# Kernel tuning notes

Hardware: AMD Instinct MI355X
Metric: run time of the kernel (lower is better)

The kernel has to match this reference:

```python
import jax, jax.numpy as jnp
import numpy as np

N_NODES = 100000
N_EDGES = 1600000
IN_FEATS = 128
HIDDEN = 128
NUM_CLASSES = 4


def setup_inputs() -> dict:
    key = jax.random.key(0)
    ks = jax.random.split(key, 8)
    features = jax.random.normal(ks[0], (N_NODES, IN_FEATS), dtype=jnp.float32)
    src = jax.random.randint(ks[1], (N_EDGES,), 0, N_NODES, dtype=jnp.int64)
    dst = jax.random.randint(ks[2], (N_EDGES,), 0, N_NODES, dtype=jnp.int64)
    s = 1.0 / np.sqrt(IN_FEATS)
    W1 = jax.random.normal(ks[3], (IN_FEATS, HIDDEN), dtype=jnp.float32) * s
    b1 = jnp.zeros((HIDDEN,), dtype=jnp.float32)
    W2 = jax.random.normal(ks[4], (HIDDEN, HIDDEN), dtype=jnp.float32) * s
    b2 = jnp.zeros((HIDDEN,), dtype=jnp.float32)
    Wc = jax.random.normal(ks[5], (HIDDEN, NUM_CLASSES), dtype=jnp.float32) * s
    bc = jnp.zeros((NUM_CLASSES,), dtype=jnp.float32)
    return {"features": features, "src": src, "dst": dst,
            "W1": W1, "b1": b1, "W2": W2, "b2": b2, "Wc": Wc, "bc": bc}


def _graph_conv(x, W, b, src, dst, n_nodes, activation=True):
    # DGL GraphConv, norm='both': D_out^{-1/2} A^T D_in... i.e. symmetric norm.
    ones = jnp.ones((src.shape[0],), dtype=x.dtype)
    deg_out = jnp.clip(jax.ops.segment_sum(ones, src, num_segments=n_nodes), 1.0)
    deg_in = jnp.clip(jax.ops.segment_sum(ones, dst, num_segments=n_nodes), 1.0)
    # scale sources, project (in >= out so matmul first, math-equivalent), gather-scatter
    h = (x * (deg_out ** -0.5)[:, None]) @ W            # [N, out]
    msg = h[src]                                         # [E, out] gather
    agg = jax.ops.segment_sum(msg, dst, num_segments=n_nodes)  # [N, out] scatter-add
    h = agg * (deg_in ** -0.5)[:, None] + b
    return jax.nn.relu(h) if activation else h


def reference(features, src, dst, W1, b1, W2, b2, Wc, bc):
    # eval-mode forward: dropout is identity
    n = features.shape[0]
    h = _graph_conv(features, W1, b1, src, dst, n, activation=True)
    h = _graph_conv(h, W2, b2, src, dst, n, activation=True)
    return h @ Wc + bc  # [N, num_classes] logits
```

## Files before the change

kernel.cpp:

```cpp
#include <hip/hip_runtime.h>
#include <hip/hip_fp16.h>
#include <math.h>

#define N_NODES 100000
#define N_EDGES 1600000
#define F 128
#define NBUK 196
#define BSH 9
#define BSZ 512
#define CAP 10240
#define NPART 392

typedef _Float16 half8 __attribute__((ext_vector_type(8)));
typedef float    f32x4 __attribute__((ext_vector_type(4)));
typedef int      i32x4 __attribute__((ext_vector_type(4)));

__global__ __launch_bounds__(256) void init_pack(int* __restrict__ curD,
                                                 int* __restrict__ curS,
                                                 _Float16* __restrict__ padrow,
                                                 const float* __restrict__ W1,
                                                 const float* __restrict__ W2,
                                                 _Float16* __restrict__ hi1,
                                                 _Float16* __restrict__ lo1,
                                                 _Float16* __restrict__ hi2,
                                                 _Float16* __restrict__ lo2)
{
    int t = threadIdx.x;
    if (blockIdx.x == 0) {
        if (t < NBUK) { curD[t] = t * CAP; curS[t] = t * CAP; }
        if (t < 16) reinterpret_cast<int4*>(padrow)[t] = make_int4(0, 0, 0, 0);
        return;
    }
    int gidx = (blockIdx.x - 1) * 256 + t;
    const float* W = (gidx < 16384) ? W1 : W2;
    _Float16* hi = (gidx < 16384) ? hi1 : hi2;
    _Float16* lo = (gidx < 16384) ? lo1 : lo2;
    int idx = gidx & 16383;
    int f = idx >> 9, r = idx & 511;
    int l = r >> 3, j = r & 7;
    int kc = f >> 3, ct = f & 7;
    int k = kc * 32 + (l >> 4) * 8 + j;
    int n = ct * 16 + (l & 15);
    float w = W[k * 128 + n];
    _Float16 h = (_Float16)w;
    hi[idx] = h;
    lo[idx] = (_Float16)(w - (float)h);
}

__global__ __launch_bounds__(512) void part_gemm1(const int* __restrict__ src,
                                                  const int* __restrict__ dst,
                                                  int* __restrict__ curD,
                                                  int* __restrict__ curS,
                                                  int* __restrict__ bukD,
                                                  unsigned short* __restrict__ bukS,
                                                  const float* __restrict__ X,
                                                  const _Float16* __restrict__ Whi,
                                                  const _Float16* __restrict__ Wlo,
                                                  _Float16* __restrict__ Y, int N)
{
    __shared__ int hd[NBUK], hs[NBUK], bd[NBUK], bs[NBUK], cd[NBUK], cs[NBUK];
    const int tid = threadIdx.x;

    if (blockIdx.x < NPART) {
        const int chunk = (((N_EDGES + NPART - 1) / NPART) + 3) & ~3;
        const int beg = blockIdx.x * chunk;
        const int end = min(beg + chunk, N_EDGES);
        if (beg >= end) return;
        if (tid < NBUK) { hd[tid] = 0; hs[tid] = 0; cd[tid] = 0; cs[tid] = 0; }
        __syncthreads();
        const int b4 = beg >> 2, e4 = end >> 2;
        const int i0 = b4 + tid, i1 = i0 + 512;
        const bool v0 = i0 < e4, v1 = i1 < e4;
        i32x4 d0 = {}, s0 = {}, d1 = {}, s1 = {};
        if (v0) {
            d0 = reinterpret_cast<const i32x4*>(dst)[i0];
            s0 = reinterpret_cast<const i32x4*>(src)[i0];
            atomicAdd(&hd[d0.x >> BSH], 1); atomicAdd(&hd[d0.y >> BSH], 1);
            atomicAdd(&hd[d0.z >> BSH], 1); atomicAdd(&hd[d0.w >> BSH], 1);
            atomicAdd(&hs[s0.x >> BSH], 1); atomicAdd(&hs[s0.y >> BSH], 1);
            atomicAdd(&hs[s0.z >> BSH], 1); atomicAdd(&hs[s0.w >> BSH], 1);
        }
        if (v1) {
            d1 = reinterpret_cast<const i32x4*>(dst)[i1];
            s1 = reinterpret_cast<const i32x4*>(src)[i1];
            atomicAdd(&hd[d1.x >> BSH], 1); atomicAdd(&hd[d1.y >> BSH], 1);
            atomicAdd(&hd[d1.z >> BSH], 1); atomicAdd(&hd[d1.w >> BSH], 1);
            atomicAdd(&hs[s1.x >> BSH], 1); atomicAdd(&hs[s1.y >> BSH], 1);
            atomicAdd(&hs[s1.z >> BSH], 1); atomicAdd(&hs[s1.w >> BSH], 1);
        }
        __syncthreads();
        if (tid < NBUK) {
            bd[tid] = hd[tid] ? atomicAdd(&curD[tid], hd[tid]) : 0;
            bs[tid] = hs[tid] ? atomicAdd(&curS[tid], hs[tid]) : 0;
        }
        __syncthreads();
        if (v0) {
            int dd[4] = { d0.x, d0.y, d0.z, d0.w };
            int ss[4] = { s0.x, s0.y, s0.z, s0.w };
            #pragma unroll
            for (int j = 0; j < 4; j++) {
                int bin = dd[j] >> BSH;
                int r = atomicAdd(&cd[bin], 1);
                bukD[bd[bin] + r] = ((dd[j] & 511) << 17) | ss[j];
                int bin2 = ss[j] >> BSH;
                int r2 = atomicAdd(&cs[bin2], 1);
                bukS[bs[bin2] + r2] = (unsigned short)(ss[j] & 511);
            }
        }
        if (v1) {
            int dd[4] = { d1.x, d1.y, d1.z, d1.w };
            int ss[4] = { s1.x, s1.y, s1.z, s1.w };
            #pragma unroll
            for (int j = 0; j < 4; j++) {
                int bin = dd[j] >> BSH;
                int r = atomicAdd(&cd[bin], 1);
                bukD[bd[bin] + r] = ((dd[j] & 511) << 17) | ss[j];
                int bin2 = ss[j] >> BSH;
                int r2 = atomicAdd(&cs[bin2], 1);
                bukS[bs[bin2] + r2] = (unsigned short)(ss[j] & 511);
            }
        }
        return;
    }

    const int l = tid & 63, w = tid >> 6;
    const int quad = l >> 4, m = l & 15;
    const int row0 = (blockIdx.x - NPART) * 256;
    const half8* Bh = reinterpret_cast<const half8*>(Whi);
    const half8* Bl = reinterpret_cast<const half8*>(Wlo);

    f32x4 acc[2][8] = {};

    for (int kc = 0; kc < 4; kc++) {
        half8 ah[2];
        #pragma unroll
        for (int rt = 0; rt < 2; rt++) {
            int grow = row0 + w * 32 + rt * 16 + m;
            float4 xa = make_float4(0.f, 0.f, 0.f, 0.f), xb = xa;
            if (grow < N) {
                const float4* Xp = reinterpret_cast<const float4*>(X) + (size_t)grow * 32 + kc * 8 + quad * 2;
                xa = Xp[0]; xb = Xp[1];
            }
            ah[rt][0] = (_Float16)xa.x; ah[rt][1] = (_Float16)xa.y;
            ah[rt][2] = (_Float16)xa.z; ah[rt][3] = (_Float16)xa.w;
            ah[rt][4] = (_Float16)xb.x; ah[rt][5] = (_Float16)xb.y;
            ah[rt][6] = (_Float16)xb.z; ah[rt][7] = (_Float16)xb.w;
        }
        #pragma unroll
        for (int ct = 0; ct < 8; ct++) {
            int f = kc * 8 + ct;
            half8 bh = Bh[f * 64 + l];
            half8 bl = Bl[f * 64 + l];
            #pragma unroll
            for (int rt = 0; rt < 2; rt++) {
                acc[rt][ct] = __builtin_amdgcn_mfma_f32_16x16x32_f16(ah[rt], bh, acc[rt][ct], 0, 0, 0);
                acc[rt][ct] = __builtin_amdgcn_mfma_f32_16x16x32_f16(ah[rt], bl, acc[rt][ct], 0, 0, 0);
            }
        }
    }

    #pragma unroll
    for (int rt = 0; rt < 2; rt++) {
        #pragma unroll
        for (int r = 0; r < 4; r++) {
            int grow = row0 + w * 32 + rt * 16 + quad * 4 + r;
            if (grow < N) {
                #pragma unroll
                for (int ct = 0; ct < 8; ct++)
                    Y[(size_t)grow * 128 + ct * 16 + m] = (_Float16)(acc[rt][ct][r]);
            }
        }
    }
}

__global__ __launch_bounds__(512) void deg_out(const unsigned short* __restrict__ bukS,
                                               const int* __restrict__ curS,
                                               float* __restrict__ sout)
{
    __shared__ int h[BSZ];
    const int tid = threadIdx.x;
    const int n0 = blockIdx.x << BSH;
    const int lo = blockIdx.x * CAP, hi = curS[blockIdx.x];
    const int cnt = hi - lo;
    h[tid] = 0;
    __syncthreads();
    const uint4* p8 = reinterpret_cast<const uint4*>(bukS + lo);
    const int nv = cnt >> 3;
    for (int j = tid; j < nv; j += 512) {
        uint4 v = p8[j];
        atomicAdd(&h[v.x & 0xFFFF], 1); atomicAdd(&h[v.x >> 16], 1);
        atomicAdd(&h[v.y & 0xFFFF], 1); atomicAdd(&h[v.y >> 16], 1);
        atomicAdd(&h[v.z & 0xFFFF], 1); atomicAdd(&h[v.z >> 16], 1);
        atomicAdd(&h[v.w & 0xFFFF], 1); atomicAdd(&h[v.w >> 16], 1);
    }
    for (int i = lo + (nv << 3) + tid; i < hi; i += 512)
        atomicAdd(&h[bukS[i]], 1);
    __syncthreads();
    int node = n0 + tid;
    if (node < N_NODES) sout[node] = rsqrtf((float)max(h[tid], 1));
}

__global__ __launch_bounds__(512) void csr_wv(const int* __restrict__ bukD,
                                              const int* __restrict__ curD,
                                              const float* __restrict__ sout,
                                              int* __restrict__ row_ptr,
                                              float* __restrict__ sin_,
                                              int* __restrict__ col,
                                              float* __restrict__ wv)
{
    __shared__ int h[BSZ], sc[BSZ], cur[BSZ];
    const int tid = threadIdx.x;
    const int n0 = blockIdx.x << BSH;
    const int lo = blockIdx.x * CAP, hi = curD[blockIdx.x];
    const int cnt = hi - lo;
    h[tid] = 0;
    __syncthreads();
    const i32x4* p4 = reinterpret_cast<const i32x4*>(bukD + lo);
    const int nv = cnt >> 2;
    for (int j = tid; j < nv; j += 512) {
        i32x4 v = p4[j];
        atomicAdd(&h[((unsigned)v.x) >> 17], 1);
        atomicAdd(&h[((unsigned)v.y) >> 17], 1);
        atomicAdd(&h[((unsigned)v.z) >> 17], 1);
        atomicAdd(&h[((unsigned)v.w) >> 17], 1);
    }
    for (int i = lo + (nv << 2) + tid; i < hi; i += 512)
        atomicAdd(&h[((unsigned)bukD[i]) >> 17], 1);
    __syncthreads();
    int own = h[tid];
    int own4 = (own + 3) & ~3;
    sc[tid] = own4;
    __syncthreads();
    for (int off = 1; off < 512; off <<= 1) {
        int u = (tid >= off) ? sc[tid - off] : 0;
        __syncthreads();
        sc[tid] += u;
        __syncthreads();
    }
    int ex = sc[tid] - own4;
    cur[tid] = ex;
    int node = n0 + tid;
    if (node < N_NODES) {
        row_ptr[2 * node]     = lo + ex;
        row_ptr[2 * node + 1] = lo + ex + own4;
        sin_[node] = rsqrtf((float)max(own, 1));
    }
    __syncthreads();
    for (int j = tid; j < nv; j += 512) {
        i32x4 v = p4[j];
        int pv[4] = { v.x, v.y, v.z, v.w };
        #pragma unroll
        for (int q = 0; q < 4; q++) {
            int p = pv[q];
            int s = p & 0x1FFFF;
            int r = atomicAdd(&cur[((unsigned)p) >> 17], 1);
            col[lo + r] = s;
            wv[lo + r]  = sout[s];
        }
    }
    for (int i = lo + (nv << 2) + tid; i < hi; i += 512) {
        int p = bukD[i];
        int s = p & 0x1FFFF;
        int r = atomicAdd(&cur[((unsigned)p) >> 17], 1);
        col[lo + r] = s;
        wv[lo + r]  = sout[s];
    }
    for (int k = own; k < own4; k++) {
        col[lo + ex + k] = N_NODES;
        wv[lo + ex + k]  = 0.f;
    }
}

#define ACCW(vv, ww) \
    a0 = fmaf(ww, (float)vv[0], a0); a1 = fmaf(ww, (float)vv[1], a1); \
    a2 = fmaf(ww, (float)vv[2], a2); a3 = fmaf(ww, (float)vv[3], a3); \
    a4 = fmaf(ww, (float)vv[4], a4); a5 = fmaf(ww, (float)vv[5], a5); \
    a6 = fmaf(ww, (float)vv[6], a6); a7 = fmaf(ww, (float)vv[7], a7);

#define ACCU(vv) \
    a0 += (float)vv[0]; a1 += (float)vv[1]; a2 += (float)vv[2]; a3 += (float)vv[3]; \
    a4 += (float)vv[4]; a5 += (float)vv[5]; a6 += (float)vv[6]; a7 += (float)vv[7];

__global__ __launch_bounds__(256) void gather_agg_s(const _Float16* __restrict__ Hh,
                                                    const int* __restrict__ row_ptr,
                                                    const int* __restrict__ col,
                                                    const float* __restrict__ wv,
                                                    const float* __restrict__ sin_,
                                                    const float* __restrict__ bias,
                                                    _Float16* __restrict__ Yh, int N)
{
    const int sub  = threadIdx.x & 15;
    const int node = blockIdx.x * 16 + (threadIdx.x >> 4);
    if (node >= N) return;
    const int beg = row_ptr[2 * node], end = row_ptr[2 * node + 1];
    const half8* __restrict__ H8 = reinterpret_cast<const half8*>(Hh);

    float a0 = 0.f, a1 = 0.f, a2 = 0.f, a3 = 0.f, a4 = 0.f, a5 = 0.f, a6 = 0.f, a7 = 0.f;
    int i = beg;
    for (; i + 8 <= end; i += 8) {
        int4 ca = *reinterpret_cast<const int4*>(col + i);
        int4 cb = *reinterpret_cast<const int4*>(col + i + 4);
        float4 wa = *reinterpret_cast<const float4*>(wv + i);
        float4 wb = *reinterpret_cast<const float4*>(wv + i + 4);
        half8 v0 = H8[((size_t)ca.x << 4) | sub];
        half8 v1 = H8[((size_t)ca.y << 4) | sub];
        half8 v2 = H8[((size_t)ca.z << 4) | sub];
        half8 v3 = H8[((size_t)ca.w << 4) | sub];
        half8 v4 = H8[((size_t)cb.x << 4) | sub];
        half8 v5 = H8[((size_t)cb.y << 4) | sub];
        half8 v6 = H8[((size_t)cb.z << 4) | sub];
        half8 v7 = H8[((size_t)cb.w << 4) | sub];
        ACCW(v0, wa.x) ACCW(v1, wa.y) ACCW(v2, wa.z) ACCW(v3, wa.w)
        ACCW(v4, wb.x) ACCW(v5, wb.y) ACCW(v6, wb.z) ACCW(v7, wb.w)
    }
    if (i < end) {
        int4 ca = *reinterpret_cast<const int4*>(col + i);
        float4 wa = *reinterpret_cast<const float4*>(wv + i);
        half8 v0 = H8[((size_t)ca.x << 4) | sub];
        half8 v1 = H8[((size_t)ca.y << 4) | sub];
        half8 v2 = H8[((size_t)ca.z << 4) | sub];
        half8 v3 = H8[((size_t)ca.w << 4) | sub];
        ACCW(v0, wa.x) ACCW(v1, wa.y) ACCW(v2, wa.z) ACCW(v3, wa.w)
    }
    float scn = sin_[node];
    const float4* B4 = reinterpret_cast<const float4*>(bias);
    float4 bA = B4[2 * sub], bB = B4[2 * sub + 1];
    half8 o;
    o[0] = (_Float16)fmaxf(fmaf(a0, scn, bA.x), 0.f);
    o[1] = (_Float16)fmaxf(fmaf(a1, scn, bA.y), 0.f);
    o[2] = (_Float16)fmaxf(fmaf(a2, scn, bA.z), 0.f);
    o[3] = (_Float16)fmaxf(fmaf(a3, scn, bA.w), 0.f);
    o[4] = (_Float16)fmaxf(fmaf(a4, scn, bB.x), 0.f);
    o[5] = (_Float16)fmaxf(fmaf(a5, scn, bB.y), 0.f);
    o[6] = (_Float16)fmaxf(fmaf(a6, scn, bB.z), 0.f);
    o[7] = (_Float16)fmaxf(fmaf(a7, scn, bB.w), 0.f);
    reinterpret_cast<half8*>(Yh)[(size_t)node * 16 + sub] = o;
}

__global__ __launch_bounds__(256) void gather_cls(const _Float16* __restrict__ Hh,
                                                  const int* __restrict__ row_ptr,
                                                  const int* __restrict__ col,
                                                  const float* __restrict__ sin_,
                                                  const float* __restrict__ bias,
                                                  const float* __restrict__ Wc,
                                                  const float* __restrict__ bc,
                                                  float* __restrict__ out, int N)
{
    __shared__ float4 Wcs[128];
    for (int t = threadIdx.x; t < 128; t += 256)
        Wcs[t] = reinterpret_cast<const float4*>(Wc)[t];
    __syncthreads();

    const int sub  = threadIdx.x & 15;
    const int node = blockIdx.x * 16 + (threadIdx.x >> 4);
    if (node >= N) return;
    const int beg = row_ptr[2 * node], end = row_ptr[2 * node + 1];
    const half8* __restrict__ H8 = reinterpret_cast<const half8*>(Hh);

    float a0 = 0.f, a1 = 0.f, a2 = 0.f, a3 = 0.f, a4 = 0.f, a5 = 0.f, a6 = 0.f, a7 = 0.f;
    int i = beg;
    for (; i + 8 <= end; i += 8) {
        int4 ca = *reinterpret_cast<const int4*>(col + i);
        int4 cb = *reinterpret_cast<const int4*>(col + i + 4);
        half8 v0 = H8[((size_t)ca.x << 4) | sub];
        half8 v1 = H8[((size_t)ca.y << 4) | sub];
        half8 v2 = H8[((size_t)ca.z << 4) | sub];
        half8 v3 = H8[((size_t)ca.w << 4) | sub];
        half8 v4 = H8[((size_t)cb.x << 4) | sub];
        half8 v5 = H8[((size_t)cb.y << 4) | sub];
        half8 v6 = H8[((size_t)cb.z << 4) | sub];
        half8 v7 = H8[((size_t)cb.w << 4) | sub];
        ACCU(v0) ACCU(v1) ACCU(v2) ACCU(v3)
        ACCU(v4) ACCU(v5) ACCU(v6) ACCU(v7)
    }
    if (i < end) {
        int4 ca = *reinterpret_cast<const int4*>(col + i);
        half8 v0 = H8[((size_t)ca.x << 4) | sub];
        half8 v1 = H8[((size_t)ca.y << 4) | sub];
        half8 v2 = H8[((size_t)ca.z << 4) | sub];
        half8 v3 = H8[((size_t)ca.w << 4) | sub];
        ACCU(v0) ACCU(v1) ACCU(v2) ACCU(v3)
    }
    float scn = sin_[node];
    const float4* B4 = reinterpret_cast<const float4*>(bias);
    float4 bA = B4[2 * sub], bB = B4[2 * sub + 1];
    float h0 = fmaxf(fmaf(a0, scn, bA.x), 0.f);
    float h1 = fmaxf(fmaf(a1, scn, bA.y), 0.f);
    float h2 = fmaxf(fmaf(a2, scn, bA.z), 0.f);
    float h3 = fmaxf(fmaf(a3, scn, bA.w), 0.f);
    float h4 = fmaxf(fmaf(a4, scn, bB.x), 0.f);
    float h5 = fmaxf(fmaf(a5, scn, bB.y), 0.f);
    float h6 = fmaxf(fmaf(a6, scn, bB.z), 0.f);
    float h7 = fmaxf(fmaf(a7, scn, bB.w), 0.f);

    float lx = 0.f, ly = 0.f, lz = 0.f, lw = 0.f;
    float4 w;
    w = Wcs[sub * 8 + 0]; lx = fmaf(h0, w.x, lx); ly = fmaf(h0, w.y, ly); lz = fmaf(h0, w.z, lz); lw = fmaf(h0, w.w, lw);
    w = Wcs[sub * 8 + 1]; lx = fmaf(h1, w.x, lx); ly = fmaf(h1, w.y, ly); lz = fmaf(h1, w.z, lz); lw = fmaf(h1, w.w, lw);
    w = Wcs[sub * 8 + 2]; lx = fmaf(h2, w.x, lx); ly = fmaf(h2, w.y, ly); lz = fmaf(h2, w.z, lz); lw = fmaf(h2, w.w, lw);
    w = Wcs[sub * 8 + 3]; lx = fmaf(h3, w.x, lx); ly = fmaf(h3, w.y, ly); lz = fmaf(h3, w.z, lz); lw = fmaf(h3, w.w, lw);
    w = Wcs[sub * 8 + 4]; lx = fmaf(h4, w.x, lx); ly = fmaf(h4, w.y, ly); lz = fmaf(h4, w.z, lz); lw = fmaf(h4, w.w, lw);
    w = Wcs[sub * 8 + 5]; lx = fmaf(h5, w.x, lx); ly = fmaf(h5, w.y, ly); lz = fmaf(h5, w.z, lz); lw = fmaf(h5, w.w, lw);
    w = Wcs[sub * 8 + 6]; lx = fmaf(h6, w.x, lx); ly = fmaf(h6, w.y, ly); lz = fmaf(h6, w.z, lz); lw = fmaf(h6, w.w, lw);
    w = Wcs[sub * 8 + 7]; lx = fmaf(h7, w.x, lx); ly = fmaf(h7, w.y, ly); lz = fmaf(h7, w.z, lz); lw = fmaf(h7, w.w, lw);

    #pragma unroll
    for (int m = 1; m < 16; m <<= 1) {
        lx += __shfl_xor(lx, m);
        ly += __shfl_xor(ly, m);
        lz += __shfl_xor(lz, m);
        lw += __shfl_xor(lw, m);
    }
    if (sub == 0) {
        float4 bcv = reinterpret_cast<const float4*>(bc)[0];
        float4 r;
        r.x = lx + bcv.x; r.y = ly + bcv.y; r.z = lz + bcv.z; r.w = lw + bcv.w;
        reinterpret_cast<float4*>(out)[node] = r;
    }
}

__global__ __launch_bounds__(256) void gemm_mfma_f16(const _Float16* __restrict__ Xh,
                                                     const _Float16* __restrict__ Whi,
                                                     const _Float16* __restrict__ Wlo,
                                                     const float* __restrict__ srow,
                                                     _Float16* __restrict__ Y, int N)
{
    const int tid = threadIdx.x;
    const int l = tid & 63, w = tid >> 6;
    const int quad = l >> 4, m = l & 15;
    const int row0 = blockIdx.x * 128;
    const half8* Bh = reinterpret_cast<const half8*>(Whi);
    const half8* Bl = reinterpret_cast<const half8*>(Wlo);

    f32x4 acc[2][8] = {};

    for (int kc = 0; kc < 4; kc++) {
        half8 a[2];
        #pragma unroll
        for (int rt = 0; rt < 2; rt++) {
            int grow = row0 + w * 32 + rt * 16 + m;
            half8 z = {};
            a[rt] = (grow < N)
                ? *reinterpret_cast<const half8*>(Xh + (size_t)grow * 128 + kc * 32 + quad * 8)
                : z;
        }
        #pragma unroll
        for (int ct = 0; ct < 8; ct++) {
            int f = kc * 8 + ct;
            half8 bh = Bh[f * 64 + l];
            half8 bl = Bl[f * 64 + l];
            #pragma unroll
            for (int rt = 0; rt < 2; rt++) {
                acc[rt][ct] = __builtin_amdgcn_mfma_f32_16x16x32_f16(a[rt], bh, acc[rt][ct], 0, 0, 0);
                acc[rt][ct] = __builtin_amdgcn_mfma_f32_16x16x32_f16(a[rt], bl, acc[rt][ct], 0, 0, 0);
            }
        }
    }

    #pragma unroll
    for (int rt = 0; rt < 2; rt++) {
        #pragma unroll
        for (int r = 0; r < 4; r++) {
            int grow = row0 + w * 32 + rt * 16 + quad * 4 + r;
            if (grow < N) {
                float s = srow[grow];
                #pragma unroll
                for (int ct = 0; ct < 8; ct++)
                    Y[(size_t)grow * 128 + ct * 16 + m] = (_Float16)(acc[rt][ct][r] * s);
            }
        }
    }
}

extern "C" void kernel_launch(void* const* d_in, const int* in_sizes, int n_in,
                              void* d_out, int out_size, void* d_ws, size_t ws_size,
                              hipStream_t stream)
{
    const float* features = (const float*)d_in[0];
    const int*   src      = (const int*)d_in[1];
    const int*   dst      = (const int*)d_in[2];
    const float* W1       = (const float*)d_in[3];
    const float* b1       = (const float*)d_in[4];
    const float* W2       = (const float*)d_in[5];
    const float* b2       = (const float*)d_in[6];
    const float* Wc       = (const float*)d_in[7];
    const float* bc       = (const float*)d_in[8];
    float* out = (float*)d_out;

    char* ws = (char*)d_ws;
    const size_t MB = 1 << 20;
    int* curD  = (int*)(ws + 0);
    int* curS  = (int*)(ws + 1024);
    _Float16* Whi1 = (_Float16*)(ws + 64 * 1024);
    _Float16* Wlo1 = (_Float16*)(ws + 96 * 1024);
    _Float16* Whi2 = (_Float16*)(ws + 128 * 1024);
    _Float16* Wlo2 = (_Float16*)(ws + 160 * 1024);
    float* sout    = (float*)(ws + 512 * 1024);
    float* sin_    = (float*)(ws + 1 * MB);
    int*   row_ptr = (int*)(ws + 2 * MB);
    int*   col     = (int*)(ws + 3 * MB);
    float* wv      = (float*)(ws + 11 * MB);
    _Float16* hMsg = (_Float16*)(ws + 25 * MB);
    int*   bukD    = (int*)(ws + 52 * MB);
    unsigned short* bukS = (unsigned short*)(ws + 60 * MB);
    _Float16* hA   = (_Float16*)(ws + 52 * MB);

    const int N = N_NODES;
    const int NGB = (N + 15) / 16;

    init_pack<<<129, 256, 0, stream>>>(curD, curS, hMsg + (size_t)N * F,
                                       W1, W2, Whi1, Wlo1, Whi2, Wlo2);

    part_gemm1<<<NPART + 391, 512, 0, stream>>>(src, dst, curD, curS, bukD, bukS,
                                                features, Whi1, Wlo1, hMsg, N);

    deg_out<<<NBUK, 512, 0, stream>>>(bukS, curS, sout);

    csr_wv<<<NBUK, 512, 0, stream>>>(bukD, curD, sout, row_ptr, sin_, col, wv);

    gather_agg_s<<<NGB, 256, 0, stream>>>(hMsg, row_ptr, col, wv, sin_, b1, hA, N);

    gemm_mfma_f16<<<(N + 127) / 128, 256, 0, stream>>>(hA, Whi2, Wlo2, sout, hMsg, N);
    gather_cls<<<NGB, 256, 0, stream>>>(hMsg, row_ptr, col, sin_, b2, Wc, bc, out, N);
}
```

Baseline: 305.6 us.

## Fuse layer-1 gather aggregation with layer-2 MFMA GEMM; double partition blocks

The layer-1 gather/aggregate kernel now stages each block's 16 aggregated fp16 rows in shared memory and immediately multiplies them by W2 using split hi/lo fp16 MFMA. This drops the separate GEMM kernel and the global write and read of the intermediate activation. The partition phase also doubles its block count so each block handles one int4 edge vector per thread instead of two, for more parallelism in bucketing. The cost is that each small block reloads the W2 fragments, and the node-count bounds checks are removed on the assumption that N is a multiple of 16.

After: 294.5 us. 1.04x faster.

```diff
diff --git a/kernel.cpp b/kernel.cpp
--- a/kernel.cpp
+++ b/kernel.cpp
@@ -9,7 +9,7 @@
 #define BSH 9
 #define BSZ 512
 #define CAP 10240
-#define NPART 392
+#define NPART 784
 
 typedef _Float16 half8 __attribute__((ext_vector_type(8)));
 typedef float    f32x4 __attribute__((ext_vector_type(4)));
@@ -17,7 +17,8 @@
 
 __global__ __launch_bounds__(256) void init_pack(int* __restrict__ curD,
                                                  int* __restrict__ curS,
-                                                 _Float16* __restrict__ padrow,
+                                                 _Float16* __restrict__ padrow1,
+                                                 _Float16* __restrict__ padrow2,
                                                  const float* __restrict__ W1,
                                                  const float* __restrict__ W2,
                                                  _Float16* __restrict__ hi1,
@@ -28,7 +29,8 @@
     int t = threadIdx.x;
     if (blockIdx.x == 0) {
         if (t < NBUK) { curD[t] = t * CAP; curS[t] = t * CAP; }
-        if (t < 16) reinterpret_cast<int4*>(padrow)[t] = make_int4(0, 0, 0, 0);
+        if (t < 16) reinterpret_cast<int4*>(padrow1)[t] = make_int4(0, 0, 0, 0);
+        else if (t >= 32 && t < 48) reinterpret_cast<int4*>(padrow2)[t - 32] = make_int4(0, 0, 0, 0);
         return;
     }
     int gidx = (blockIdx.x - 1) * 256 + t;
@@ -69,9 +71,9 @@
         if (tid < NBUK) { hd[tid] = 0; hs[tid] = 0; cd[tid] = 0; cs[tid] = 0; }
         __syncthreads();
         const int b4 = beg >> 2, e4 = end >> 2;
-        const int i0 = b4 + tid, i1 = i0 + 512;
-        const bool v0 = i0 < e4, v1 = i1 < e4;
-        i32x4 d0 = {}, s0 = {}, d1 = {}, s1 = {};
+        const int i0 = b4 + tid;
+        const bool v0 = i0 < e4;
+        i32x4 d0 = {}, s0 = {};
         if (v0) {
             d0 = reinterpret_cast<const i32x4*>(dst)[i0];
             s0 = reinterpret_cast<const i32x4*>(src)[i0];
@@ -80,14 +82,6 @@
             atomicAdd(&hs[s0.x >> BSH], 1); atomicAdd(&hs[s0.y >> BSH], 1);
             atomicAdd(&hs[s0.z >> BSH], 1); atomicAdd(&hs[s0.w >> BSH], 1);
         }
-        if (v1) {
-            d1 = reinterpret_cast<const i32x4*>(dst)[i1];
-            s1 = reinterpret_cast<const i32x4*>(src)[i1];
-            atomicAdd(&hd[d1.x >> BSH], 1); atomicAdd(&hd[d1.y >> BSH], 1);
-            atomicAdd(&hd[d1.z >> BSH], 1); atomicAdd(&hd[d1.w >> BSH], 1);
-            atomicAdd(&hs[s1.x >> BSH], 1); atomicAdd(&hs[s1.y >> BSH], 1);
-            atomicAdd(&hs[s1.z >> BSH], 1); atomicAdd(&hs[s1.w >> BSH], 1);
-        }
         __syncthreads();
         if (tid < NBUK) {
             bd[tid] = hd[tid] ? atomicAdd(&curD[tid], hd[tid]) : 0;
@@ -97,19 +91,6 @@
         if (v0) {
             int dd[4] = { d0.x, d0.y, d0.z, d0.w };
             int ss[4] = { s0.x, s0.y, s0.z, s0.w };
-            #pragma unroll
-            for (int j = 0; j < 4; j++) {
-                int bin = dd[j] >> BSH;
-                int r = atomicAdd(&cd[bin], 1);
-                bukD[bd[bin] + r] = ((dd[j] & 511) << 17) | ss[j];
-                int bin2 = ss[j] >> BSH;
-                int r2 = atomicAdd(&cs[bin2], 1);
-                bukS[bs[bin2] + r2] = (unsigned short)(ss[j] & 511);
-            }
-        }
-        if (v1) {
-            int dd[4] = { d1.x, d1.y, d1.z, d1.w };
-            int ss[4] = { s1.x, s1.y, s1.z, s1.w };
             #pragma unroll
             for (int j = 0; j < 4; j++) {
                 int bin = dd[j] >> BSH;
@@ -281,17 +262,22 @@
     a0 += (float)vv[0]; a1 += (float)vv[1]; a2 += (float)vv[2]; a3 += (float)vv[3]; \
     a4 += (float)vv[4]; a5 += (float)vv[5]; a6 += (float)vv[6]; a7 += (float)vv[7];
 
-__global__ __launch_bounds__(256) void gather_agg_s(const _Float16* __restrict__ Hh,
+__global__ __launch_bounds__(256) void gather_gemm2(const _Float16* __restrict__ Hh,
                                                     const int* __restrict__ row_ptr,
                                                     const int* __restrict__ col,
                                                     const float* __restrict__ wv,
                                                     const float* __restrict__ sin_,
                                                     const float* __restrict__ bias,
-                                                    _Float16* __restrict__ Yh, int N)
-{
-    const int sub  = threadIdx.x & 15;
-    const int node = blockIdx.x * 16 + (threadIdx.x >> 4);
-    if (node >= N) return;
+                                                    const _Float16* __restrict__ Whi,
+                                                    const _Float16* __restrict__ Wlo,
+                                                    const float* __restrict__ sout,
+                                                    _Float16* __restrict__ Y)
+{
+    __shared__ _Float16 At[16][128];
+    const int tid = threadIdx.x;
+    const int sub  = tid & 15;
+    const int g0   = tid >> 4;
+    const int node = blockIdx.x * 16 + g0;
     const int beg = row_ptr[2 * node], end = row_ptr[2 * node + 1];
     const half8* __restrict__ H8 = reinterpret_cast<const half8*>(Hh);
 
@@ -322,19 +308,52 @@
         half8 v3 = H8[((size_t)ca.w << 4) | sub];
         ACCW(v0, wa.x) ACCW(v1, wa.y) ACCW(v2, wa.z) ACCW(v3, wa.w)
     }
-    float scn = sin_[node];
-    const float4* B4 = reinterpret_cast<const float4*>(bias);
-    float4 bA = B4[2 * sub], bB = B4[2 * sub + 1];
-    half8 o;
-    o[0] = (_Float16)fmaxf(fmaf(a0, scn, bA.x), 0.f);
-    o[1] = (_Float16)fmaxf(fmaf(a1, scn, bA.y), 0.f);
-    o[2] = (_Float16)fmaxf(fmaf(a2, scn, bA.z), 0.f);
-    o[3] = (_Float16)fmaxf(fmaf(a3, scn, bA.w), 0.f);
-    o[4] = (_Float16)fmaxf(fmaf(a4, scn, bB.x), 0.f);
-    o[5] = (_Float16)fmaxf(fmaf(a5, scn, bB.y), 0.f);
-    o[6] = (_Float16)fmaxf(fmaf(a6, scn, bB.z), 0.f);
-    o[7] = (_Float16)fmaxf(fmaf(a7, scn, bB.w), 0.f);
-    reinterpret_cast<half8*>(Yh)[(size_t)node * 16 + sub] = o;
+    {
+        float scn = sin_[node];
+        const float4* B4 = reinterpret_cast<const float4*>(bias);
+        float4 bA = B4[2 * sub], bB = B4[2 * sub + 1];
+        half8 o;
+        o[0] = (_Float16)fmaxf(fmaf(a0, scn, bA.x), 0.f);
+        o[1] = (_Float16)fmaxf(fmaf(a1, scn, bA.y), 0.f);
+        o[2] = (_Float16)fmaxf(fmaf(a2, scn, bA.z), 0.f);
+        o[3] = (_Float16)fmaxf(fmaf(a3, scn, bA.w), 0.f);
+        o[4] = (_Float16)fmaxf(fmaf(a4, scn, bB.x), 0.f);
+        o[5] = (_Float16)fmaxf(fmaf(a5, scn, bB.y), 0.f);
+        o[6] = (_Float16)fmaxf(fmaf(a6, scn, bB.z), 0.f);
+        o[7] = (_Float16)fmaxf(fmaf(a7, scn, bB.w), 0.f);
+        *reinterpret_cast<half8*>(&At[g0][sub * 8]) = o;
+    }
+    __syncthreads();
+
+    const int l = tid & 63, w = tid >> 6;
+    const int quad = l >> 4, m = l & 15;
+    const half8* Bh = reinterpret_cast<const half8*>(Whi);
+    const half8* Bl = reinterpret_cast<const half8*>(Wlo);
+
+    f32x4 acc0 = {}, acc1 = {};
+    #pragma unroll
+    for (int kc = 0; kc < 4; kc++) {
+        half8 a = *reinterpret_cast<const half8*>(&At[m][kc * 32 + quad * 8]);
+        int f0 = kc * 8 + w * 2;
+        half8 bh0 = Bh[f0 * 64 + l];
+        half8 bl0 = Bl[f0 * 64 + l];
+        half8 bh1 = Bh[(f0 + 1) * 64 + l];
+        half8 bl1 = Bl[(f0 + 1) * 64 + l];
+        acc0 = __builtin_amdgcn_mfma_f32_16x16x32_f16(a, bh0, acc0, 0, 0, 0);
+        acc0 = __builtin_amdgcn_mfma_f32_16x16x32_f16(a, bl0, acc0, 0, 0, 0);
+        acc1 = __builtin_amdgcn_mfma_f32_16x16x32_f16(a, bh1, acc1, 0, 0, 0);
+        acc1 = __builtin_amdgcn_mfma_f32_16x16x32_f16(a, bl1, acc1, 0, 0, 0);
+    }
+
+    const int rbase = blockIdx.x * 16 + quad * 4;
+    const int c0 = (w * 2) * 16 + m;
+    #pragma unroll
+    for (int r = 0; r < 4; r++) {
+        int grow = rbase + r;
+        float s = sout[grow];
+        Y[(size_t)grow * 128 + c0]      = (_Float16)(acc0[r] * s);
+        Y[(size_t)grow * 128 + c0 + 16] = (_Float16)(acc1[r] * s);
+    }
 }
 
 __global__ __launch_bounds__(256) void gather_cls(const _Float16* __restrict__ Hh,
@@ -416,59 +435,6 @@
         float4 r;
         r.x = lx + bcv.x; r.y = ly + bcv.y; r.z = lz + bcv.z; r.w = lw + bcv.w;
         reinterpret_cast<float4*>(out)[node] = r;
-    }
-}
-
-__global__ __launch_bounds__(256) void gemm_mfma_f16(const _Float16* __restrict__ Xh,
-                                                     const _Float16* __restrict__ Whi,
-                                                     const _Float16* __restrict__ Wlo,
-                                                     const float* __restrict__ srow,
-                                                     _Float16* __restrict__ Y, int N)
-{
-    const int tid = threadIdx.x;
-    const int l = tid & 63, w = tid >> 6;
-    const int quad = l >> 4, m = l & 15;
-    const int row0 = blockIdx.x * 128;
-    const half8* Bh = reinterpret_cast<const half8*>(Whi);
-    const half8* Bl = reinterpret_cast<const half8*>(Wlo);
-
-    f32x4 acc[2][8] = {};
-
-    for (int kc = 0; kc < 4; kc++) {
-        half8 a[2];
-        #pragma unroll
-        for (int rt = 0; rt < 2; rt++) {
-            int grow = row0 + w * 32 + rt * 16 + m;
-            half8 z = {};
-            a[rt] = (grow < N)
-                ? *reinterpret_cast<const half8*>(Xh + (size_t)grow * 128 + kc * 32 + quad * 8)
-                : z;
-        }
-        #pragma unroll
-        for (int ct = 0; ct < 8; ct++) {
-            int f = kc * 8 + ct;
-            half8 bh = Bh[f * 64 + l];
-            half8 bl = Bl[f * 64 + l];
-            #pragma unroll
-            for (int rt = 0; rt < 2; rt++) {
-                acc[rt][ct] = __builtin_amdgcn_mfma_f32_16x16x32_f16(a[rt], bh, acc[rt][ct], 0, 0, 0);
-                acc[rt][ct] = __builtin_amdgcn_mfma_f32_16x16x32_f16(a[rt], bl, acc[rt][ct], 0, 0, 0);
-            }
-        }
-    }
-
-    #pragma unroll
-    for (int rt = 0; rt < 2; rt++) {
-        #pragma unroll
-        for (int r = 0; r < 4; r++) {
-            int grow = row0 + w * 32 + rt * 16 + quad * 4 + r;
-            if (grow < N) {
-                float s = srow[grow];
-                #pragma unroll
-                for (int ct = 0; ct < 8; ct++)
-                    Y[(size_t)grow * 128 + ct * 16 + m] = (_Float16)(acc[rt][ct][r] * s);
-            }
-        }
     }
 }
 
@@ -508,7 +474,8 @@
     const int N = N_NODES;
     const int NGB = (N + 15) / 16;
 
-    init_pack<<<129, 256, 0, stream>>>(curD, curS, hMsg + (size_t)N * F,
+    init_pack<<<129, 256, 0, stream>>>(curD, curS,
+                                       hMsg + (size_t)N * F, hA + (size_t)N * F,
                                        W1, W2, Whi1, Wlo1, Whi2, Wlo2);
 
     part_gemm1<<<NPART + 391, 512, 0, stream>>>(src, dst, curD, curS, bukD, bukS,
@@ -518,8 +485,8 @@
 
     csr_wv<<<NBUK, 512, 0, stream>>>(bukD, curD, sout, row_ptr, sin_, col, wv);
 
-    gather_agg_s<<<NGB, 256, 0, stream>>>(hMsg, row_ptr, col, wv, sin_, b1, hA, N);
-
-    gemm_mfma_f16<<<(N + 127) / 128, 256, 0, stream>>>(hA, Whi2, Wlo2, sout, hMsg, N);
-    gather_cls<<<NGB, 256, 0, stream>>>(hMsg, row_ptr, col, sin_, b2, Wc, bc, out, N);
-}
+    gather_gemm2<<<NGB, 256, 0, stream>>>(hMsg, row_ptr, col, wv, sin_, b1,
+                                          Whi2, Wlo2, sout, hA);
+
+    gather_cls<<<NGB, 256, 0, stream>>>(hA, row_ptr, col, sin_, b2, Wc, bc, out, N);
+}
```
